# Kernel tuning notes

Measured on AMD Instinct MI355X. Metric: run time of the kernel, lower is better.

Reference implementation:

```python
import jax, jax.numpy as jnp
import numpy as np
from jax import lax

NEG = -1e30  # log-space 'zero' (avoid -inf for mixed-precision safety)
EPS = 1e-7   # keras backend epsilon used in ctc_batch_cost


def setup_inputs() -> dict:
    key = jax.random.key(0)
    k1, k2 = jax.random.split(key)
    B, T, L, V = 64, 1024, 128, 512
    # labels in [0, V-2]; blank index is V-1 (keras ctc_batch_cost convention)
    y_true = jax.random.randint(k1, (B, L), 0, V - 1, dtype=jnp.int64)
    # y_pred are softmax probabilities (ctc_batch_cost logs them internally)
    y_pred = jax.random.uniform(k2, (B, T, V), dtype=jnp.float32)
    y_pred = y_pred / jnp.sum(y_pred, axis=-1, keepdims=True)
    return {"y_true": y_true, "y_pred": y_pred}


def _ctc_loss(y_true, y_pred):
    # y_true: [B, L] int labels; y_pred: [B, T, V] probabilities
    B, T, V = y_pred.shape
    L = y_true.shape[1]
    blank = V - 1
    S = 2 * L + 1  # extended label length: blank,l1,blank,l2,...,blank

    logp = jnp.log(y_pred + EPS)  # [B, T, V]

    # extended label sequence per batch row
    ext = jnp.full((B, S), blank, dtype=y_true.dtype)
    ext = ext.at[:, 1::2].set(y_true)  # [B, S]

    # gather log-probs of extended labels at every time step -> [B, T, S]
    idx = jnp.broadcast_to(ext[:, None, :], (B, T, S))
    lp = jnp.take_along_axis(logp, idx, axis=2)

    # skip transition s-2 -> s allowed iff ext[s] != blank and ext[s] != ext[s-2]
    prev2 = jnp.concatenate([jnp.full((B, 2), -1, dtype=ext.dtype), ext[:, :-2]], axis=1)
    allow_skip = (ext != blank) & (ext != prev2)  # [B, S]

    # init alpha at t=0: only states 0 (blank) and 1 (first label) reachable
    alpha0 = jnp.full((B, S), NEG, dtype=logp.dtype)
    alpha0 = alpha0.at[:, 0].set(lp[:, 0, 0]).at[:, 1].set(lp[:, 0, 1])

    pad1 = jnp.full((B, 1), NEG, dtype=logp.dtype)
    pad2 = jnp.full((B, 2), NEG, dtype=logp.dtype)

    def step(alpha, lp_t):  # alpha, lp_t: [B, S]
        a1 = jnp.concatenate([pad1, alpha[:, :-1]], axis=1)
        a2 = jnp.concatenate([pad2, alpha[:, :-2]], axis=1)
        a2 = jnp.where(allow_skip, a2, NEG)
        new = jnp.logaddexp(jnp.logaddexp(alpha, a1), a2) + lp_t
        return new, None

    lp_rest = jnp.moveaxis(lp[:, 1:], 1, 0)  # [T-1, B, S], time-major for scan
    alpha_T, _ = lax.scan(step, alpha0, lp_rest)

    # total prob ends in last blank or last label
    log_p = jnp.logaddexp(alpha_T[:, -1], alpha_T[:, -2])  # [B]
    return -log_p[:, None]  # [B, 1] like keras ctc_batch_cost


def reference(y_true, y_pred):
    return _ctc_loss(y_true, y_pred)
```

## Files before the change

### kernel.cpp

```cpp
#include <hip/hip_runtime.h>
#include <hip/hip_bf16.h>
#include <cstdint>


#define CTC_B 64
#define CTC_T 1024
#define CTC_L 128
#define CTC_V 512
#define BLANK (CTC_V - 1)
#define EPSF 1e-7f
#define LN2F 0.69314718055994530942f
#define BIASE 90
#define K1ROWS 16

typedef __attribute__((ext_vector_type(4))) unsigned int u32x4;
typedef __attribute__((ext_vector_type(4))) float f32x4;

__device__ __forceinline__ void gld_lds16f(const float* g, float* l) {
    __builtin_amdgcn_global_load_lds(
        (const __attribute__((address_space(1))) unsigned int*)g,
        (__attribute__((address_space(3))) unsigned int*)l, 16, 0, 0);
}

template<int CTRL>
__device__ __forceinline__ float dpp_mov0(float v) {
    int r = __builtin_amdgcn_update_dpp(0, __float_as_int(v), CTRL, 0xf, 0xf, false);
    return __int_as_float(r);
}
template<int CTRL>
__device__ __forceinline__ float dpp_max(float v) {
    int r = __builtin_amdgcn_update_dpp(__float_as_int(v), __float_as_int(v),
                                        CTRL, 0xf, 0xf, false);
    return fmaxf(v, __int_as_float(r));
}
__device__ __forceinline__ uint32_t rne16(float x) {
    return (__float_as_uint(x) + 0x8000u) >> 16;
}

__global__ __launch_bounds__(256, 1)
void ctc_gather(const int* __restrict__ y_true,
                const float* __restrict__ y_pred,
                uint32_t* __restrict__ pairs,
                float* __restrict__ blk) {
    __shared__ __align__(16) float rows[K1ROWS][CTC_V];

    const int bid = blockIdx.x;
    const int b = bid >> 6;
    const int t0 = (bid & 63) * K1ROWS;
    const int w = threadIdx.x >> 6;
    const int lane = threadIdx.x & 63;
    const float* __restrict__ yb = y_pred + ((size_t)b * CTC_T + t0) * CTC_V;

    const int2 lp = *(const int2*)&y_true[b * CTC_L + 2 * lane];

#pragma unroll
    for (int r = 0; r < 4; ++r) {
        const int row = 4 * w + r;
        const float* g = yb + (size_t)row * CTC_V + lane * 4;
        gld_lds16f(g, &rows[row][0]);
        gld_lds16f(g + 256, &rows[row][256]);
    }
    asm volatile("s_waitcnt vmcnt(0)" ::: "memory");

    uint32_t pk0, pk1, pk2, pk3;
    float bl0, bl1, bl2, bl3;
#define PACKROW(R) do {                                                    \
        const float* rowp = &rows[4 * w + (R)][0];                         \
        pk##R = rne16(rowp[lp.x] + EPSF) | (rne16(rowp[lp.y] + EPSF) << 16); \
        bl##R = rowp[BLANK] + EPSF;                                        \
    } while (0)
    PACKROW(0); PACKROW(1); PACKROW(2); PACKROW(3);
#undef PACKROW

    const size_t gidx = ((size_t)b * CTC_T + t0) / 4 + w;
    u32x4 pv; pv.x = pk0; pv.y = pk1; pv.z = pk2; pv.w = pk3;
    ((u32x4*)pairs)[gidx * 64 + lane] = pv;
    if (lane == 0) {
        f32x4 bv; bv.x = bl0; bv.y = bl1; bv.z = bl2; bv.w = bl3;
        ((f32x4*)blk)[gidx] = bv;
    }
}

#define GLD4U(dst, addr, OFF)                                              \
    asm volatile("global_load_dwordx4 %0, %1, off offset:" OFF             \
                 : "=v"(dst) : "v"(addr) : "memory")
#define GLD4F(dst, addr, OFF)                                              \
    asm volatile("global_load_dwordx4 %0, %1, off offset:" OFF             \
                 : "=v"(dst) : "v"(addr) : "memory")

__global__ __launch_bounds__(64, 1)
void ctc_scan3(const int* __restrict__ y_true,
               const uint32_t* __restrict__ pairs,
               const float* __restrict__ blk,
               float* __restrict__ out) {
    const int b = blockIdx.x;
    const int lane = threadIdx.x;

    const uint8_t* pbase = (const uint8_t*)pairs + (size_t)b * 262144 + (size_t)lane * 16;
    const uint8_t* bbase = (const uint8_t*)blk + (size_t)b * 4096;

    const int labA = y_true[b * CTC_L + 2 * lane];
    const int labB = y_true[b * CTC_L + 2 * lane + 1];
    const int labPrev = __shfl_up(labB, 1);
    const float msk1 = (labA != labPrev) ? 1.0f : 0.0f;
    const float msk3 = (labB != labA) ? 1.0f : 0.0f;

    float a0 = (lane == 0) ? 1.0f : 0.0f;
    float a1 = 0.0f, a2 = 0.0f, a3 = 0.0f, a4 = 0.0f;
    float curScale = 1.0f;
    int curE = 0, Eacc = 0;

    u32x4 PA0, PA1, PA2, PA3, PA4, PA5, PA6, PA7;
    f32x4 QA0, QA1, QA2, QA3, QA4, QA5, QA6, QA7;
    u32x4 PB0, PB1, PB2, PB3, PB4, PB5, PB6, PB7;
    f32x4 QB0, QB1, QB2, QB3, QB4, QB5, QB6, QB7;

#define ISSUE_PHASE(S) do {                                                \
        const uint8_t* ph_ = pbase + 4096;                                 \
        GLD4U(P##S##0, pbase, "0");    GLD4U(P##S##1, pbase, "1024");      \
        GLD4U(P##S##2, pbase, "2048"); GLD4U(P##S##3, pbase, "3072");      \
        GLD4U(P##S##4, ph_,   "0");    GLD4U(P##S##5, ph_,   "1024");      \
        GLD4U(P##S##6, ph_,   "2048"); GLD4U(P##S##7, ph_,   "3072");      \
        GLD4F(Q##S##0, bbase, "0");    GLD4F(Q##S##1, bbase, "16");        \
        GLD4F(Q##S##2, bbase, "32");   GLD4F(Q##S##3, bbase, "48");        \
        GLD4F(Q##S##4, bbase, "64");   GLD4F(Q##S##5, bbase, "80");        \
        GLD4F(Q##S##6, bbase, "96");   GLD4F(Q##S##7, bbase, "112");       \
        pbase += 8192; bbase += 128;                                       \
    } while (0)

#define WAITP() do {                                                       \
        asm volatile("s_waitcnt vmcnt(16)" ::: "memory");                  \
        __builtin_amdgcn_sched_barrier(0);                                 \
    } while (0)

#define STEP(vk, bv) do {                                                  \
        const float pb_ = (bv);                                            \
        const float pA_ = __uint_as_float((vk) << 16);                     \
        const float pB_ = __uint_as_float((vk) & 0xffff0000u);             \
        const float pm1_ = dpp_mov0<0x138>(a3);  \
        const float n0_ = (a0 + pm1_) * pb_;                               \
        const float n1_ = fmaf(msk1, pm1_, a0 + a1) * pA_;                 \
        const float n2_ = (a1 + a2) * pb_;                                 \
        const float n3_ = fmaf(msk3, a1, a2 + a3) * pB_;                   \
        const float n4_ = (a3 + a4) * pb_;                                 \
        a0 = n0_; a1 = n1_; a2 = n2_; a3 = n3_; a4 = n4_;                  \
    } while (0)

#define DORN() do {                                                        \
        a0 *= curScale; a1 *= curScale; a2 *= curScale;                    \
        a3 *= curScale; a4 *= curScale;                                    \
        Eacc += curE;                                                      \
        float m_ = fmaxf(fmaxf(fmaxf(a0, a1), fmaxf(a2, a3)), a4);         \
        m_ = dpp_max<0x111>(m_);                           \
        m_ = dpp_max<0x112>(m_);                           \
        m_ = dpp_max<0x114>(m_);                           \
        m_ = dpp_max<0x118>(m_);                           \
        m_ = dpp_max<0x142>(m_);                         \
        m_ = dpp_max<0x143>(m_);                         \
        const int mb_ = __builtin_amdgcn_readlane(__float_as_int(m_), 63); \
        const int e_ = (mb_ >> 23) & 255;                                  \
        int k_ = 127 + BIASE + 127 - e_;                                   \
        k_ = k_ > 254 ? 254 : (k_ < 1 ? 1 : k_);                           \
        curScale = __int_as_float((unsigned)k_ << 23);                     \
        curE = 127 - k_;                                                   \
    } while (0)

#define GROUPSTEP(S, G) do {                                               \
        STEP(P##S##G.x, Q##S##G.x);                                        \
        STEP(P##S##G.y, Q##S##G.y);                                        \
        STEP(P##S##G.z, Q##S##G.z);                                        \
        STEP(P##S##G.w, Q##S##G.w);                                        \
        DORN();                                                            \
    } while (0)

#define PROC_PHASE(S) do {                                                 \
        GROUPSTEP(S, 0); GROUPSTEP(S, 1); GROUPSTEP(S, 2); GROUPSTEP(S, 3);\
        GROUPSTEP(S, 4); GROUPSTEP(S, 5); GROUPSTEP(S, 6); GROUPSTEP(S, 7);\
    } while (0)

    ISSUE_PHASE(A);
    for (int it = 0; it < 16; ++it) {
        ISSUE_PHASE(B);
        WAITP();
        PROC_PHASE(A);
        ISSUE_PHASE(A);
        WAITP();
        PROC_PHASE(B);
    }

    if (lane == 63) {
        out[b] = -(logf(a3 + a4) + (float)Eacc * LN2F);
    }
#undef PROC_PHASE
#undef GROUPSTEP
#undef DORN
#undef STEP
#undef WAITP
#undef ISSUE_PHASE
}
#undef GLD4U
#undef GLD4F

#define F_CHUNK 16
#define F_NBUF  4
#define F_NCH   (CTC_T / F_CHUNK)

__global__ __launch_bounds__(256, 1)
void ctc_fwd_stream(const int* __restrict__ y_true,
                    const float* __restrict__ y_pred,
                    float* __restrict__ out) {
    __shared__ __align__(16) float rows[F_NBUF][F_CHUNK][CTC_V];
    const int b = blockIdx.x;
    const int tid = threadIdx.x;
    const int wave = tid >> 6;
    const int lane = tid & 63;
    const float* __restrict__ yb = y_pred + (size_t)b * CTC_T * CTC_V;

    if (wave != 0) {
        const int w = wave - 1;
#define FISSUE(c_) do {                                                    \
            const int t0_ = (c_) * F_CHUNK;                                \
            float* bufb_ = &rows[(c_) & (F_NBUF - 1)][0][0];               \
            for (int l_ = w; l_ < F_CHUNK; l_ += 3) {                      \
                const float* g_ = yb + (size_t)(t0_ + l_) * CTC_V + lane * 4; \
                float* d_ = bufb_ + l_ * CTC_V;                            \
                gld_lds16f(g_, d_);                                        \
                gld_lds16f(g_ + 256, d_ + 256);                            \
            }                                                              \
        } while (0)
        FISSUE(0); FISSUE(1); FISSUE(2);
        if (w == 0) asm volatile("s_waitcnt vmcnt(24)" ::: "memory");
        else        asm volatile("s_waitcnt vmcnt(20)" ::: "memory");
        __builtin_amdgcn_s_barrier();
        __builtin_amdgcn_sched_barrier(0);
        for (int c = 0; c < F_NCH; ++c) {
            if (c + 3 < F_NCH) FISSUE(c + 3);
            if (c <= F_NCH - 4) {
                if (w == 0) asm volatile("s_waitcnt vmcnt(24)" ::: "memory");
                else        asm volatile("s_waitcnt vmcnt(20)" ::: "memory");
            } else if (c == F_NCH - 3) {
                if (w == 0) asm volatile("s_waitcnt vmcnt(12)" ::: "memory");
                else        asm volatile("s_waitcnt vmcnt(10)" ::: "memory");
            } else if (c == F_NCH - 2) {
                asm volatile("s_waitcnt vmcnt(0)" ::: "memory");
            }
            __builtin_amdgcn_s_barrier();
            __builtin_amdgcn_sched_barrier(0);
        }
        return;
#undef FISSUE
    }

    const int labA = y_true[b * CTC_L + 2 * lane];
    const int labB = y_true[b * CTC_L + 2 * lane + 1];
    const int labPrev = __shfl_up(labB, 1);
    const float msk1 = (labA != labPrev) ? 1.0f : 0.0f;
    const float msk3 = (labB != labA) ? 1.0f : 0.0f;

    float a0 = 0.0f, a1 = 0.0f, a2 = 0.0f, a3 = 0.0f, a4 = 0.0f;
    float curScale = 1.0f;
    int curE = 0, Eacc = 0;
    float pAA0, pBA0, blA0, pAA1, pBA1, blA1, pAA2, pBA2, blA2, pAA3, pBA3, blA3;
    float pAB0, pBB0, blB0, pAB1, pBB1, blB1, pAB2, pBB2, blB2, pAB3, pBB3, blB3;
    float pAC0, pBC0, blC0, pAC1, pBC1, blC1, pAC2, pBC2, blC2, pAC3, pBC3, blC3;

#define FLOADG(S, l_) do {                                                 \
        const float* r0_ = bufc + ((l_) + 0) * CTC_V;                      \
        const float* r1_ = bufc + ((l_) + 1) * CTC_V;                      \
        const float* r2_ = bufc + ((l_) + 2) * CTC_V;                      \
        const float* r3_ = bufc + ((l_) + 3) * CTC_V;                      \
        pA##S##0 = r0_[labA]; pB##S##0 = r0_[labB]; bl##S##0 = r0_[BLANK]; \
        pA##S##1 = r1_[labA]; pB##S##1 = r1_[labB]; bl##S##1 = r1_[BLANK]; \
        pA##S##2 = r2_[labA]; pB##S##2 = r2_[labB]; bl##S##2 = r2_[BLANK]; \
        pA##S##3 = r3_[labA]; pB##S##3 = r3_[labB]; bl##S##3 = r3_[BLANK]; \
    } while (0)
#define FDOSTEP(S, k) do {                                                 \
        const float pb_ = bl##S##k + EPSF;                                 \
        const float pA_ = pA##S##k + EPSF;                                 \
        const float pB_ = pB##S##k + EPSF;                                 \
        const float pm1_ = dpp_mov0<0x138>(a3);                            \
        const float n0_ = (a0 + pm1_) * pb_;                               \
        const float n1_ = fmaf(msk1, pm1_, a0 + a1) * pA_;                 \
        const float n2_ = (a1 + a2) * pb_;                                 \
        const float n3_ = fmaf(msk3, a1, a2 + a3) * pB_;                   \
        const float n4_ = (a3 + a4) * pb_;                                 \
        a0 = n0_; a1 = n1_; a2 = n2_; a3 = n3_; a4 = n4_;                  \
    } while (0)
#define FDORN() do {                                                       \
        a0 *= curScale; a1 *= curScale; a2 *= curScale;                    \
        a3 *= curScale; a4 *= curScale;                                    \
        Eacc += curE;                                                      \
        float m_ = fmaxf(fmaxf(fmaxf(a0, a1), fmaxf(a2, a3)), a4);         \
        m_ = dpp_max<0x111>(m_); m_ = dpp_max<0x112>(m_);                  \
        m_ = dpp_max<0x114>(m_); m_ = dpp_max<0x118>(m_);                  \
        m_ = dpp_max<0x142>(m_); m_ = dpp_max<0x143>(m_);                  \
        const int mb_ = __builtin_amdgcn_readlane(__float_as_int(m_), 63); \
        const int e_ = (mb_ >> 23) & 255;                                  \
        int k_ = 127 + BIASE + 127 - e_;                                   \
        k_ = k_ > 254 ? 254 : (k_ < 1 ? 1 : k_);                           \
        curScale = __int_as_float((unsigned)k_ << 23);                     \
        curE = 127 - k_;                                                   \
    } while (0)
#define FPROC4_RN(S) do {                                                  \
        FDOSTEP(S, 0); FDORN();                                            \
        FDOSTEP(S, 1); FDOSTEP(S, 2); FDOSTEP(S, 3);                       \
    } while (0)

    __builtin_amdgcn_s_barrier();
    __builtin_amdgcn_sched_barrier(0);
    for (int c = 0; c < F_NCH; ++c) {
        const float* bufc = &rows[c & (F_NBUF - 1)][0][0];
        if (c == 0) {
            const float pb0 = bufc[BLANK] + EPSF;
            const float plA = bufc[labA] + EPSF;
            FLOADG(A, 0); FLOADG(B, 4); FLOADG(C, 8);
            a0 = (lane == 0) ? pb0 : 0.0f;
            a1 = (lane == 0) ? plA : 0.0f;
            FDOSTEP(A, 1); FDOSTEP(A, 2); FDOSTEP(A, 3);
            FLOADG(A, 12);
            FPROC4_RN(B); FPROC4_RN(C); FPROC4_RN(A);
        } else {
            FLOADG(A, 0); FLOADG(B, 4); FLOADG(C, 8);
            FPROC4_RN(A); FLOADG(A, 12);
            FPROC4_RN(B); FPROC4_RN(C); FPROC4_RN(A);
        }
        __builtin_amdgcn_s_barrier();
        __builtin_amdgcn_sched_barrier(0);
    }
    if (lane == 63) {
        out[b] = -(logf(a3 + a4) + (float)Eacc * LN2F);
    }
#undef FPROC4_RN
#undef FDORN
#undef FDOSTEP
#undef FLOADG
}

extern "C" void kernel_launch(void* const* d_in, const int* in_sizes, int n_in,
                              void* d_out, int out_size, void* d_ws, size_t ws_size,
                              hipStream_t stream) {
    (void)in_sizes; (void)n_in; (void)out_size;
    const int* y_true = (const int*)d_in[0];
    const float* y_pred = (const float*)d_in[1];
    float* out = (float*)d_out;

    const size_t pairsBytes = (size_t)CTC_B * CTC_T * 64 * sizeof(uint32_t);
    const size_t blkBytes = (size_t)CTC_B * CTC_T * sizeof(float);
    const size_t need = pairsBytes + blkBytes + 65536;
    if (ws_size >= need) {
        uint32_t* pairs = (uint32_t*)d_ws;
        float* blk = (float*)((char*)d_ws + pairsBytes);
        ctc_gather<<<CTC_B * (CTC_T / K1ROWS), 256, 0, stream>>>(y_true, y_pred, pairs, blk);
        ctc_scan3<<<CTC_B, 64, 0, stream>>>(y_true, pairs, blk, out);
    } else {
        ctc_fwd_stream<<<CTC_B, 256, 0, stream>>>(y_true, y_pred, out);
    }
}
```

Before: 78.75 us.

## Interleave two batch rows per wave in the CTC scan kernel

The scan kernel now has each 64-lane block process two batch rows (b and b+32) at once, interleaving their alpha recurrences step by step. It launches half as many blocks. The aim is to give the latency-bound serial recurrence two independent dependency chains, so DPP/FMA latency and load latency can be overlapped. In exchange each wave does twice the work with more registers, and only 32 CUs are used, so any latency that is not hidden adds directly to total time.

```diff
diff --git a/kernel.cpp b/kernel.cpp
--- a/kernel.cpp
+++ b/kernel.cpp
@@ -81,51 +81,57 @@
     }
 }
 
-#define GLD4U(dst, addr, OFF)                                              \
+#define GLD4(dst, addr, OFF)                                               \
     asm volatile("global_load_dwordx4 %0, %1, off offset:" OFF             \
                  : "=v"(dst) : "v"(addr) : "memory")
-#define GLD4F(dst, addr, OFF)                                              \
-    asm volatile("global_load_dwordx4 %0, %1, off offset:" OFF             \
-                 : "=v"(dst) : "v"(addr) : "memory")
 
 __global__ __launch_bounds__(64, 1)
-void ctc_scan3(const int* __restrict__ y_true,
+void ctc_scan4(const int* __restrict__ y_true,
                const uint32_t* __restrict__ pairs,
                const float* __restrict__ blk,
                float* __restrict__ out) {
-    const int b = blockIdx.x;
+    const int b0 = blockIdx.x;
+    const int b1 = b0 + CTC_B / 2;
     const int lane = threadIdx.x;
 
-    const uint8_t* pbase = (const uint8_t*)pairs + (size_t)b * 262144 + (size_t)lane * 16;
-    const uint8_t* bbase = (const uint8_t*)blk + (size_t)b * 4096;
-
-    const int labA = y_true[b * CTC_L + 2 * lane];
-    const int labB = y_true[b * CTC_L + 2 * lane + 1];
-    const int labPrev = __shfl_up(labB, 1);
-    const float msk1 = (labA != labPrev) ? 1.0f : 0.0f;
-    const float msk3 = (labB != labA) ? 1.0f : 0.0f;
-
-    float a0 = (lane == 0) ? 1.0f : 0.0f;
-    float a1 = 0.0f, a2 = 0.0f, a3 = 0.0f, a4 = 0.0f;
-    float curScale = 1.0f;
-    int curE = 0, Eacc = 0;
-
-    u32x4 PA0, PA1, PA2, PA3, PA4, PA5, PA6, PA7;
-    f32x4 QA0, QA1, QA2, QA3, QA4, QA5, QA6, QA7;
-    u32x4 PB0, PB1, PB2, PB3, PB4, PB5, PB6, PB7;
-    f32x4 QB0, QB1, QB2, QB3, QB4, QB5, QB6, QB7;
+    const uint8_t* px = (const uint8_t*)pairs + (size_t)b0 * 262144 + (size_t)lane * 16;
+    const uint8_t* py = (const uint8_t*)pairs + (size_t)b1 * 262144 + (size_t)lane * 16;
+    const uint8_t* bx = (const uint8_t*)blk + (size_t)b0 * 4096;
+    const uint8_t* by = (const uint8_t*)blk + (size_t)b1 * 4096;
+
+    const int labAX = y_true[b0 * CTC_L + 2 * lane];
+    const int labBX = y_true[b0 * CTC_L + 2 * lane + 1];
+    const int labPX = __shfl_up(labBX, 1);
+    const float msk1X = (labAX != labPX) ? 1.0f : 0.0f;
+    const float msk3X = (labBX != labAX) ? 1.0f : 0.0f;
+    const int labAY = y_true[b1 * CTC_L + 2 * lane];
+    const int labBY = y_true[b1 * CTC_L + 2 * lane + 1];
+    const int labPY = __shfl_up(labBY, 1);
+    const float msk1Y = (labAY != labPY) ? 1.0f : 0.0f;
+    const float msk3Y = (labBY != labAY) ? 1.0f : 0.0f;
+
+    float aX0 = (lane == 0) ? 1.0f : 0.0f;
+    float aX1 = 0.0f, aX2 = 0.0f, aX3 = 0.0f, aX4 = 0.0f;
+    float aY0 = (lane == 0) ? 1.0f : 0.0f;
+    float aY1 = 0.0f, aY2 = 0.0f, aY3 = 0.0f, aY4 = 0.0f;
+    float curScaleX = 1.0f, curScaleY = 1.0f;
+    int curEX = 0, EaccX = 0, curEY = 0, EaccY = 0;
+
+    u32x4 PXA0, PXA1, PXA2, PXA3, PXB0, PXB1, PXB2, PXB3;
+    u32x4 PYA0, PYA1, PYA2, PYA3, PYB0, PYB1, PYB2, PYB3;
+    f32x4 QXA0, QXA1, QXA2, QXA3, QXB0, QXB1, QXB2, QXB3;
+    f32x4 QYA0, QYA1, QYA2, QYA3, QYB0, QYB1, QYB2, QYB3;
 
 #define ISSUE_PHASE(S) do {                                                \
-        const uint8_t* ph_ = pbase + 4096;                                 \
-        GLD4U(P##S##0, pbase, "0");    GLD4U(P##S##1, pbase, "1024");      \
-        GLD4U(P##S##2, pbase, "2048"); GLD4U(P##S##3, pbase, "3072");      \
-        GLD4U(P##S##4, ph_,   "0");    GLD4U(P##S##5, ph_,   "1024");      \
-        GLD4U(P##S##6, ph_,   "2048"); GLD4U(P##S##7, ph_,   "3072");      \
-        GLD4F(Q##S##0, bbase, "0");    GLD4F(Q##S##1, bbase, "16");        \
-        GLD4F(Q##S##2, bbase, "32");   GLD4F(Q##S##3, bbase, "48");        \
-        GLD4F(Q##S##4, bbase, "64");   GLD4F(Q##S##5, bbase, "80");        \
-        GLD4F(Q##S##6, bbase, "96");   GLD4F(Q##S##7, bbase, "112");       \
-        pbase += 8192; bbase += 128;                                       \
+        GLD4(PX##S##0, px, "0");    GLD4(PX##S##1, px, "1024");            \
+        GLD4(PX##S##2, px, "2048"); GLD4(PX##S##3, px, "3072");            \
+        GLD4(PY##S##0, py, "0");    GLD4(PY##S##1, py, "1024");            \
+        GLD4(PY##S##2, py, "2048"); GLD4(PY##S##3, py, "3072");            \
+        GLD4(QX##S##0, bx, "0");    GLD4(QX##S##1, bx, "16");              \
+        GLD4(QX##S##2, bx, "32");   GLD4(QX##S##3, bx, "48");              \
+        GLD4(QY##S##0, by, "0");    GLD4(QY##S##1, by, "16");              \
+        GLD4(QY##S##2, by, "32");   GLD4(QY##S##3, by, "48");              \
+        px += 4096; py += 4096; bx += 64; by += 64;                        \
     } while (0)
 
 #define WAITP() do {                                                       \
@@ -133,24 +139,27 @@
         __builtin_amdgcn_sched_barrier(0);                                 \
     } while (0)
 
-#define STEP(vk, bv) do {                                                  \
+#define STEPR(R, vk, bv) do {                                              \
         const float pb_ = (bv);                                            \
         const float pA_ = __uint_as_float((vk) << 16);                     \
         const float pB_ = __uint_as_float((vk) & 0xffff0000u);             \
-        const float pm1_ = dpp_mov0<0x138>(a3);  \
-        const float n0_ = (a0 + pm1_) * pb_;                               \
-        const float n1_ = fmaf(msk1, pm1_, a0 + a1) * pA_;                 \
-        const float n2_ = (a1 + a2) * pb_;                                 \
-        const float n3_ = fmaf(msk3, a1, a2 + a3) * pB_;                   \
-        const float n4_ = (a3 + a4) * pb_;                                 \
-        a0 = n0_; a1 = n1_; a2 = n2_; a3 = n3_; a4 = n4_;                  \
-    } while (0)
-
-#define DORN() do {                                                        \
-        a0 *= curScale; a1 *= curScale; a2 *= curScale;                    \
-        a3 *= curScale; a4 *= curScale;                                    \
-        Eacc += curE;                                                      \
-        float m_ = fmaxf(fmaxf(fmaxf(a0, a1), fmaxf(a2, a3)), a4);         \
+        const float pm1_ = dpp_mov0<0x138>(a##R##3);       \
+        const float n0_ = (a##R##0 + pm1_) * pb_;                          \
+        const float n1_ = fmaf(msk1##R, pm1_, a##R##0 + a##R##1) * pA_;    \
+        const float n2_ = (a##R##1 + a##R##2) * pb_;                       \
+        const float n3_ = fmaf(msk3##R, a##R##1, a##R##2 + a##R##3) * pB_; \
+        const float n4_ = (a##R##3 + a##R##4) * pb_;                       \
+        a##R##0 = n0_; a##R##1 = n1_; a##R##2 = n2_;                       \
+        a##R##3 = n3_; a##R##4 = n4_;                                      \
+    } while (0)
+
+#define DORNR(R) do {                                                      \
+        a##R##0 *= curScale##R; a##R##1 *= curScale##R;                    \
+        a##R##2 *= curScale##R; a##R##3 *= curScale##R;                    \
+        a##R##4 *= curScale##R;                                            \
+        Eacc##R += curE##R;                                                \
+        float m_ = fmaxf(fmaxf(fmaxf(a##R##0, a##R##1),                    \
+                               fmaxf(a##R##2, a##R##3)), a##R##4);         \
         m_ = dpp_max<0x111>(m_);                           \
         m_ = dpp_max<0x112>(m_);                           \
         m_ = dpp_max<0x114>(m_);                           \
@@ -161,25 +170,24 @@
         const int e_ = (mb_ >> 23) & 255;                                  \
         int k_ = 127 + BIASE + 127 - e_;                                   \
         k_ = k_ > 254 ? 254 : (k_ < 1 ? 1 : k_);                           \
-        curScale = __int_as_float((unsigned)k_ << 23);                     \
-        curE = 127 - k_;                                                   \
-    } while (0)
-
-#define GROUPSTEP(S, G) do {                                               \
-        STEP(P##S##G.x, Q##S##G.x);                                        \
-        STEP(P##S##G.y, Q##S##G.y);                                        \
-        STEP(P##S##G.z, Q##S##G.z);                                        \
-        STEP(P##S##G.w, Q##S##G.w);                                        \
-        DORN();                                                            \
+        curScale##R = __int_as_float((unsigned)k_ << 23);                  \
+        curE##R = 127 - k_;                                                \
+    } while (0)
+
+#define GROUP(S, G) do {                                                   \
+        STEPR(X, PX##S##G.x, QX##S##G.x); STEPR(Y, PY##S##G.x, QY##S##G.x);\
+        STEPR(X, PX##S##G.y, QX##S##G.y); STEPR(Y, PY##S##G.y, QY##S##G.y);\
+        STEPR(X, PX##S##G.z, QX##S##G.z); STEPR(Y, PY##S##G.z, QY##S##G.z);\
+        STEPR(X, PX##S##G.w, QX##S##G.w); STEPR(Y, PY##S##G.w, QY##S##G.w);\
+        DORNR(X); DORNR(Y);                                                \
     } while (0)
 
 #define PROC_PHASE(S) do {                                                 \
-        GROUPSTEP(S, 0); GROUPSTEP(S, 1); GROUPSTEP(S, 2); GROUPSTEP(S, 3);\
-        GROUPSTEP(S, 4); GROUPSTEP(S, 5); GROUPSTEP(S, 6); GROUPSTEP(S, 7);\
+        GROUP(S, 0); GROUP(S, 1); GROUP(S, 2); GROUP(S, 3);                \
     } while (0)
 
     ISSUE_PHASE(A);
-    for (int it = 0; it < 16; ++it) {
+    for (int it = 0; it < 32; ++it) {
         ISSUE_PHASE(B);
         WAITP();
         PROC_PHASE(A);
@@ -189,17 +197,17 @@
     }
 
     if (lane == 63) {
-        out[b] = -(logf(a3 + a4) + (float)Eacc * LN2F);
+        out[b0] = -(logf(aX3 + aX4) + (float)EaccX * LN2F);
+        out[b1] = -(logf(aY3 + aY4) + (float)EaccY * LN2F);
     }
 #undef PROC_PHASE
-#undef GROUPSTEP
-#undef DORN
-#undef STEP
+#undef GROUP
+#undef DORNR
+#undef STEPR
 #undef WAITP
 #undef ISSUE_PHASE
 }
-#undef GLD4U
-#undef GLD4F
+#undef GLD4
 
 #define F_CHUNK 16
 #define F_NBUF  4
@@ -351,7 +359,7 @@
         uint32_t* pairs = (uint32_t*)d_ws;
         float* blk = (float*)((char*)d_ws + pairsBytes);
         ctc_gather<<<CTC_B * (CTC_T / K1ROWS), 256, 0, stream>>>(y_true, y_pred, pairs, blk);
-        ctc_scan3<<<CTC_B, 64, 0, stream>>>(y_true, pairs, blk, out);
+        ctc_scan4<<<CTC_B / 2, 64, 0, stream>>>(y_true, pairs, blk, out);
     } else {
         ctc_fwd_stream<<<CTC_B, 256, 0, stream>>>(y_true, y_pred, out);
     }
```

New measurement: 128.2 us. +62.8%, slower.
